# Kernel tuning notes

Measured on AMD Instinct MI355X. Metric: run time of the kernel, lower is better.

Reference implementation:

```python
import jax, jax.numpy as jnp
import numpy as np

SR = 48000
NC = 8      # num_cylinders
NH = 64     # num_harmonics
NB = 32     # num_noisebands
B_, T_ = 2, 65536
TWO_PI = 2.0 * np.pi


def _gumbel_softmax_hard(key, logits, tau=1.0):
    g = jax.random.gumbel(key, logits.shape, dtype=logits.dtype)
    y = jax.nn.softmax((logits + g) / tau)
    hard = jax.nn.one_hot(jnp.argmax(y, axis=-1), logits.shape[-1], dtype=y.dtype)
    return hard + y - jax.lax.stop_gradient(y)  # straight-through (hard=True)


def _resonant_activation(x, min_mag):
    return jnp.sign(x) * (min_mag + (1.0 - min_mag) * jnp.abs(jnp.tanh(x)))


def _format_coefficients(one_hot, fb_gain, refl, lowpass, tau):
    shifted = jnp.roll(one_hot, 1, axis=-1)
    refl = jax.nn.sigmoid(refl) if lowpass else jnp.tanh(refl)
    k1 = _resonant_activation(refl[0], tau)
    k2 = _resonant_activation(refl[1], tau)
    a1 = k1 * (1.0 - k2)
    a2 = jnp.clip(k2, -0.999, 0.999)
    a1_bound = 0.999 - jnp.abs(a2)
    a1 = jnp.clip(a1, -a1_bound, a1_bound)
    g = jax.nn.sigmoid(fb_gain[0]) ** 0.45
    return one_hot * (a1 * g) + shifted * (a2 * g)


def _sample_wise_lpc(x, a):
    # All-pole IIR: y[t] = x[t] - sum_{i=1..P} a[t, i-1] * y[t-i]
    # x: (B,T), a: (B,T,P) -> (B,T). Inherently sequential scan over T.
    B, T = x.shape
    P = a.shape[-1]

    def step(buf, inp):          # buf: (B,P) = [y[t-1], ..., y[t-P]]
        xt, at = inp             # (B,), (B,P)
        yt = xt - jnp.sum(at * buf, axis=-1)
        buf = jnp.concatenate([yt[:, None], buf[:, :-1]], axis=1)
        return buf, yt

    buf0 = jnp.zeros((B, P), x.dtype)
    _, y = jax.lax.scan(step, buf0, (x.T, jnp.transpose(a, (1, 0, 2))))
    return y.T


def _resonator(excitation, delay_param, fb_gain, refl, min_delay, max_delay, lowpass, tau, key):
    # excitation: (B,1,T)
    sel = _gumbel_softmax_hard(key, delay_param)                 # (max-min,)
    coeffs = _format_coefficients(sel, fb_gain, refl, lowpass, tau)
    coeffs = jnp.concatenate([jnp.zeros(min_delay, coeffs.dtype), coeffs])  # (max_delay,)
    x = excitation[:, 0, :]
    B, T = x.shape
    a = jnp.broadcast_to(coeffs[None, None, :], (B, T, max_delay))
    return _sample_wise_lpc(x, a)[:, None, :]


def setup_inputs() -> dict:
    key = jax.random.key(0)
    ks = jax.random.split(key, 16)
    inp = {
        'f0': jax.random.uniform(ks[0], (B_, 1, T_), jnp.float32),
        'harmonic_amplitudes': jax.random.uniform(ks[1], (B_, NC * NH, T_), jnp.float32),
        'harmonic_fm': jax.random.uniform(ks[2], (B_, 1, T_), jnp.float32),
        'cylinder_phase_offsets': jax.random.normal(ks[3], (B_, NC, T_), jnp.float32),
        'cylinder_pulse_shapes': jax.random.uniform(ks[4], (B_, 2 * NC, T_), jnp.float32),
        'noisebank_amplitudes': jax.random.uniform(ks[5], (B_, NB, T_), jnp.float32),
        'noise_pulse_shapes': jax.random.uniform(ks[6], (B_, 2, T_), jnp.float32),
        'noise_pulse_gain': jax.random.uniform(ks[7], (B_, 1, T_), jnp.float32),
        'flow_noise_gain': jax.random.uniform(ks[8], (B_, 1, T_), jnp.float32),
        'noise_bands': jax.random.normal(ks[9], (NB, T_), jnp.float32),
        'delay_a': jax.random.normal(ks[10], (125 - 40,), jnp.float32),
        'fbgain_a': jnp.ones((1,), jnp.float32),
        'refl_a': jax.random.normal(ks[11], (2,), jnp.float32),
        'delay_b': jax.random.normal(ks[12], (125 - 40,), jnp.float32),
        'fbgain_b': jnp.ones((1,), jnp.float32),
        'refl_b': jax.random.normal(ks[13], (2,), jnp.float32),
        'delay_c': jax.random.normal(ks[14], (40 - 32,), jnp.float32),
        'fbgain_c': jnp.ones((1,), jnp.float32),
        'refl_c': jax.random.normal(ks[15], (2,), jnp.float32),
    }
    return inp


def reference(f0, harmonic_amplitudes, harmonic_fm, cylinder_phase_offsets,
              cylinder_pulse_shapes, noisebank_amplitudes, noise_pulse_shapes,
              noise_pulse_gain, flow_noise_gain, noise_bands,
              delay_a, fbgain_a, refl_a, delay_b, fbgain_b, refl_b,
              delay_c, fbgain_c, refl_c):
    B, C, T = cylinder_phase_offsets.shape
    firing_order = jnp.array([0, 4, 3, 7, 5, 2, 6, 1], dtype=f0.dtype)[:NC]
    firing_angles = firing_order / NC * TWO_PI                         # (8,)
    power_cycle_phase = jnp.cumsum(TWO_PI * f0 / SR, axis=-1) * 0.5    # (B,1,T)
    cylinder_phases = (power_cycle_phase + firing_angles[None, :, None]) % TWO_PI  # (B,8,T)

    hp = (cylinder_phases / TWO_PI) ** harmonic_fm                     # (B,8,T)
    hp = hp * TWO_PI
    harm_idx = jnp.arange(1, NH + 1, dtype=hp.dtype)
    osc = -jnp.sin(hp[:, :, None, :] * harm_idx[None, None, :, None])  # (B,8,64,T)
    amps = harmonic_amplitudes.reshape(B, NC, NH, T)
    harmonics = jnp.sum(osc * amps, axis=2)                            # (B,8,T)

    cyl_alpha = cylinder_pulse_shapes[:, :NC, :]
    cyl_beta = cylinder_pulse_shapes[:, NC:, :]
    cyl_env = (1.0 - jnp.exp(-cyl_alpha * cylinder_phases)) * jnp.exp(-cyl_beta * cylinder_phases)
    harmonics = harmonics * cyl_env * 10.0

    # NoiseBank: fixed noise bands weighted per-sample and summed over bands
    noise = jnp.einsum('bnt,nt->bt', noisebank_amplitudes, noise_bands)[:, None, :]  # (B,1,T)

    n_alpha = noise_pulse_shapes[:, 0:1, :]
    n_beta = noise_pulse_shapes[:, 1:2, :]
    noise_phase = power_cycle_phase % TWO_PI
    noise_env = (1.0 - jnp.exp(-n_alpha * noise_phase)) * jnp.exp(-n_beta * noise_phase)
    noise_bursts = noise * noise_env * noise_pulse_gain
    flow_noise = noise * flow_noise_gain * 0.3
    turbulence = harmonics * noise * (noise_pulse_gain + flow_noise_gain) * 0.7
    cylinders = harmonics + noise_bursts + flow_noise + turbulence     # (B,8,T)

    bank_a = jnp.sum(cylinders[:, :4, :], axis=1, keepdims=True)       # (B,1,T)
    bank_b = jnp.sum(cylinders[:, 4:, :], axis=1, keepdims=True)

    ka, kb, kc = jax.random.split(jax.random.key(42), 3)
    res_a = _resonator(bank_a, delay_a, fbgain_a, refl_a, 40, 125, False, 0.0, ka)
    res_b = _resonator(bank_b, delay_b, fbgain_b, refl_b, 40, 125, False, 0.0, kb)
    res_c = _resonator(res_a + res_b, delay_c, fbgain_c, refl_c, 32, 40, True, 0.0, kc)
    return jnp.sum(res_c, axis=1, keepdims=True)                       # (B,1,T)
```

## Files before the change

### kernel.cpp

```cpp
#include <hip/hip_runtime.h>
#include <cstdint>
#include <cstddef>

#define T_ 65536

__device__ __forceinline__ void tf2x32(uint32_t k0, uint32_t k1,
                                       uint32_t& x0, uint32_t& x1) {
  const uint32_t ks[3] = {k0, k1, k0 ^ k1 ^ 0x1BD11BDAu};
  const int R[8] = {13, 15, 26, 6, 17, 29, 16, 24};
  x0 += ks[0]; x1 += ks[1];
#pragma unroll
  for (int i = 0; i < 5; ++i) {
#pragma unroll
    for (int j = 0; j < 4; ++j) {
      const int r = R[(i & 1) * 4 + j];
      x0 += x1;
      x1 = (x1 << r) | (x1 >> (32 - r));
      x1 ^= x0;
    }
    x0 += ks[(i + 1) % 3];
    x1 += ks[(i + 2) % 3] + (uint32_t)(i + 1);
  }
}

__device__ __forceinline__ float gumbel_from_bits(uint32_t b) {
  float u = __uint_as_float((b >> 9) | 0x3f800000u) - 1.0f;
  u = fmaxf(u, 1.17549435e-38f);
  return -logf(-logf(u));
}

__global__ __launch_bounds__(1024) void pcp_coef_kernel(
    const float* __restrict__ f0, float* __restrict__ pcp,
    const float* __restrict__ da, const float* __restrict__ fa, const float* __restrict__ ra,
    const float* __restrict__ db, const float* __restrict__ fb, const float* __restrict__ rb,
    const float* __restrict__ dc, const float* __restrict__ fc, const float* __restrict__ rc,
    float* __restrict__ cws) {
  __shared__ double sm[1024];
  __shared__ float z[128];
  if (blockIdx.x < 2) {
    const int b = blockIdx.x;
    const int tid = threadIdx.x;
    const float* src = f0 + (size_t)b * T_;
    const int base = tid * 64;
    double loc = 0.0;
#pragma unroll 4
    for (int k = 0; k < 16; ++k) {
      const float4 a = *(const float4*)(src + base + 4 * k);
      loc += 6.283185307179586 * (double)a.x / 48000.0;
      loc += 6.283185307179586 * (double)a.y / 48000.0;
      loc += 6.283185307179586 * (double)a.z / 48000.0;
      loc += 6.283185307179586 * (double)a.w / 48000.0;
    }
    sm[tid] = loc;
    __syncthreads();
    for (int off = 1; off < 1024; off <<= 1) {
      double v = (tid >= off) ? sm[tid - off] : 0.0;
      __syncthreads();
      sm[tid] += v;
      __syncthreads();
    }
    double run = (tid > 0) ? sm[tid - 1] : 0.0;
    float* dst = pcp + (size_t)b * T_;
#pragma unroll 4
    for (int k = 0; k < 16; ++k) {
      const float4 a = *(const float4*)(src + base + 4 * k);
      const double r0 = run + 6.283185307179586 * (double)a.x / 48000.0;
      const double r1 = r0  + 6.283185307179586 * (double)a.y / 48000.0;
      const double r2 = r1  + 6.283185307179586 * (double)a.z / 48000.0;
      const double r3 = r2  + 6.283185307179586 * (double)a.w / 48000.0;
      *(float4*)(dst + base + 4 * k) = make_float4((float)(r0 * 0.5), (float)(r1 * 0.5),
                                                   (float)(r2 * 0.5), (float)(r3 * 0.5));
      run = r3;
    }
  } else {
    uint32_t keys[3][2];
#pragma unroll
    for (int q = 0; q < 3; ++q) {
      uint32_t x0 = 0u, x1 = (uint32_t)q;
      tf2x32(0u, 42u, x0, x1);
      keys[q][0] = x0; keys[q][1] = x1;
    }
    const float* dl[3] = {da, db, dc};
    const float* fg[3] = {fa, fb, fc};
    const float* rf[3] = {ra, rb, rc};
    const int Ls[3] = {85, 85, 8};
    const int md[3] = {40, 40, 32};
    const int i = threadIdx.x;
    for (int r = 0; r < 3; ++r) {
      const int L = Ls[r];
      if (i < 128) z[i] = -3.4e38f;
      __syncthreads();
      if (i < L) {
        uint32_t x0 = 0u, x1 = (uint32_t)i;
        tf2x32(keys[r][0], keys[r][1], x0, x1);
        z[i] = dl[r][i] + gumbel_from_bits(x0 ^ x1);
      }
      __syncthreads();
      if (i == 0) {
        int p = 0; float best = z[0];
        for (int j = 1; j < L; ++j) { float v = z[j]; if (v > best) { best = v; p = j; } }
        const bool lowpass = (r == 2);
        float r0 = rf[r][0], r1 = rf[r][1];
        if (lowpass) { r0 = 1.f / (1.f + expf(-r0)); r1 = 1.f / (1.f + expf(-r1)); }
        else         { r0 = tanhf(r0);               r1 = tanhf(r1); }
        const float k1 = tanhf(r0), k2 = tanhf(r1);
        float a1 = k1 * (1.f - k2);
        const float a2 = fminf(fmaxf(k2, -0.999f), 0.999f);
        const float bnd = 0.999f - fabsf(a2);
        a1 = fminf(fmaxf(a1, -bnd), bnd);
        const float g = powf(1.f / (1.f + expf(-fg[r][0])), 0.45f);
        const int D1 = md[r] + p + 1;
        const int D2 = md[r] + ((p + 1) % L) + 1;
        const float C1 = a1 * g;
        const float C2 = a2 * g;
        float* cw = cws + r * 32;
        const float bin4[5] = {1.f, 4.f, 6.f, 4.f, 1.f};
        const float c1p[5] = {1.f, C1, C1*C1, C1*C1*C1, C1*C1*C1*C1};
        const float c2p[5] = {1.f, C2, C2*C2, C2*C2*C2, C2*C2*C2*C2};
        for (int j = 0; j < 5; ++j) {
          cw[j]     = (float)((4 - j) * D1 + j * D2);
          cw[5 + j] = bin4[j] * c1p[4 - j] * c2p[j];
        }
        const int   fd[9] = {D1, D2, 2*D1, D1+D2, 2*D2, 3*D1, 2*D1+D2, D1+2*D2, 3*D2};
        const float fn[9] = {-C1, -C2, C1*C1, 2.f*C1*C2, C2*C2,
                             -C1*C1*C1, -3.f*C1*C1*C2, -3.f*C1*C2*C2, -C2*C2*C2};
        for (int k = 0; k < 9; ++k) {
          cw[10 + k] = (float)fd[k];
          cw[19 + k] = fn[k];
        }
      }
      __syncthreads();
    }
  }
}

__global__ __launch_bounds__(256) void synth_kernel(
    const float* __restrict__ amps,
    const float* __restrict__ fmg,
    const float* __restrict__ cps,
    const float* __restrict__ nba,
    const float* __restrict__ nps,
    const float* __restrict__ npg,
    const float* __restrict__ fng,
    const float* __restrict__ bands,
    const float* __restrict__ pcp,
    float* __restrict__ bank_a, float* __restrict__ bank_b) {
  const float TPF = 6.283185307179586f;
  const int lane = threadIdx.x & 63;
  const int g    = threadIdx.x >> 6;
  const int blk  = blockIdx.x;
  const int b    = blk >> 8;
  const int t    = (blk & 255) * 256 + lane * 4;
  const size_t bt = (size_t)b * T_ + t;

  __shared__ float4 redN[4][64];
  __shared__ float4 redH[4][64];

  const float4 p4 = *(const float4*)(pcp + bt);
  const float4 f4 = *(const float4*)(fmg + bt);

  float4 nse = make_float4(0.f, 0.f, 0.f, 0.f);
#pragma unroll
  for (int j = 0; j < 8; ++j) {
    const int n = g * 8 + j;
    const float4 a = *(const float4*)(nba + ((size_t)b * 32 + n) * T_ + t);
    const float4 w = *(const float4*)(bands + (size_t)n * T_ + t);
    nse.x += a.x * w.x; nse.y += a.y * w.y;
    nse.z += a.z * w.z; nse.w += a.w * w.w;
  }
  redN[g][lane] = nse;

  const int order[8] = {0, 4, 3, 7, 5, 2, 6, 1};
  float4 hp = make_float4(0.f, 0.f, 0.f, 0.f);
#pragma unroll
  for (int cc = 0; cc < 2; ++cc) {
    const int c = 2 * g + cc;
    const float ang = ((float)order[c] / 8.0f) * TPF;
#define SETUP(C_)                                                     \
    float s##C_ = p4.C_ + ang; if (s##C_ >= TPF) s##C_ -= TPF;        \
    float sn##C_, cs##C_;                                             \
    sincosf(TPF * powf(s##C_ / TPF, f4.C_), &sn##C_, &cs##C_);        \
    float sp##C_ = 0.f, sc##C_ = sn##C_;                              \
    const float tc##C_ = 2.f * cs##C_;                                \
    float acc##C_ = 0.f;
    SETUP(x) SETUP(y) SETUP(z) SETUP(w)
#undef SETUP
    const float* ap = amps + ((size_t)b * 512 + (size_t)c * 64) * T_ + t;
#pragma unroll 4
    for (int h = 0; h < 64; ++h) {
      const float4 a = *(const float4*)(ap + (size_t)h * T_);
#define HSTEP(C_) {                                                   \
      acc##C_ += a.C_ * sc##C_;                                       \
      const float nx = tc##C_ * sc##C_ - sp##C_;                      \
      sp##C_ = sc##C_; sc##C_ = nx; }
      HSTEP(x) HSTEP(y) HSTEP(z) HSTEP(w)
#undef HSTEP
    }
    const float4 al = *(const float4*)(cps + ((size_t)b * 16 + c) * T_ + t);
    const float4 be = *(const float4*)(cps + ((size_t)b * 16 + 8 + c) * T_ + t);
#define ENVACC(C_) {                                                  \
      const float env = (1.f - expf(-al.C_ * s##C_)) * expf(-be.C_ * s##C_); \
      hp.C_ += -acc##C_ * env * 10.f; }
    ENVACC(x) ENVACC(y) ENVACC(z) ENVACC(w)
#undef ENVACC
  }
  redH[g][lane] = hp;
  __syncthreads();

  if (g == 0) {
    const float4 nA = redN[0][lane], nB = redN[1][lane],
                 nC = redN[2][lane], nD = redN[3][lane];
    const float4 hA0 = redH[0][lane], hA1 = redH[1][lane],
                 hB0 = redH[2][lane], hB1 = redH[3][lane];
    const float4 g4  = *(const float4*)(npg + bt);
    const float4 fl4 = *(const float4*)(fng + bt);
    const float4 na4 = *(const float4*)(nps + (size_t)b * 2 * T_ + t);
    const float4 nb4 = *(const float4*)(nps + ((size_t)b * 2 + 1) * T_ + t);
    float4 outA, outB;
#define FIN(C_) {                                                     \
    const float nse = nA.C_ + nB.C_ + nC.C_ + nD.C_;                  \
    const float ha = hA0.C_ + hA1.C_;                                 \
    const float hb = hB0.C_ + hB1.C_;                                 \
    float q = p4.C_; if (q >= TPF) q -= TPF;                          \
    const float ne = (1.f - expf(-na4.C_ * q)) * expf(-nb4.C_ * q);   \
    const float com = nse * (ne * g4.C_ + fl4.C_ * 0.3f);             \
    const float K = nse * (g4.C_ + fl4.C_) * 0.7f;                    \
    outA.C_ = ha * (1.f + K) + 4.f * com;                             \
    outB.C_ = hb * (1.f + K) + 4.f * com; }
    FIN(x) FIN(y) FIN(z) FIN(w)
#undef FIN
    *(float4*)(bank_a + bt) = outA;
    *(float4*)(bank_b + bt) = outB;
  }
}

__global__ __launch_bounds__(256) void prep_ab_kernel(
    const float* __restrict__ BA, const float* __restrict__ BB,
    const float* __restrict__ CW, float* __restrict__ XA, float* __restrict__ XB) {
  const int idx = blockIdx.x * 256 + threadIdx.x;
  const int t = idx & (T_ - 1);
  const int s = idx >> 16;
  const int r = s >> 1, b = s & 1;
  const float* xin = (r == 0 ? BA : BB) + (size_t)b * T_;
  float* xout = (r == 0 ? XA : XB) + (size_t)b * T_;
  const float* cw = CW + r * 32;
  float acc = xin[t];
#pragma unroll
  for (int k = 0; k < 9; ++k) {
    const int d = (int)cw[10 + k];
    const float n = cw[19 + k];
    const int tc = t - d;
    const float u = xin[tc >= 0 ? tc : 0];
    acc += (tc >= 0) ? n * u : 0.f;
  }
  xout[t] = acc;
}

__global__ __launch_bounds__(256) void prep_c_kernel(
    const float* __restrict__ RA, const float* __restrict__ RB,
    const float* __restrict__ CW, float* __restrict__ XC) {
  const int idx = blockIdx.x * 256 + threadIdx.x;
  const int t = idx & (T_ - 1);
  const int b = idx >> 16;
  const float* ya = RA + (size_t)b * T_;
  const float* yb = RB + (size_t)b * T_;
  const float* cw = CW + 64;
  float acc = ya[t] + yb[t];
#pragma unroll
  for (int k = 0; k < 9; ++k) {
    const int d = (int)cw[10 + k];
    const float n = cw[19 + k];
    const int tc = t - d;
    const float u = ya[tc >= 0 ? tc : 0] + yb[tc >= 0 ? tc : 0];
    acc += (tc >= 0) ? n * u : 0.f;
  }
  XC[idx] = acc;
}

__device__ __forceinline__ void gld16(const float* g, float* l) {
  __builtin_amdgcn_global_load_lds((const __attribute__((address_space(1))) void*)g,
                                   (__attribute__((address_space(3))) void*)l, 16, 0, 0);
}

__device__ __forceinline__ void poly_scan(const float* __restrict__ x,
                                          float* __restrict__ y,
                                          const float* __restrict__ cf,
                                          float* __restrict__ sm) {
  const int o = threadIdx.x & 63;
  const int e0 = (int)cf[0], e1 = (int)cf[1], e2 = (int)cf[2],
            e3 = (int)cf[3], e4 = (int)cf[4];
  const float fc0 = cf[5], fc1 = cf[6], fc2 = cf[7], fc3 = cf[8], fc4 = cf[9];
  float* ring = sm;
  float* st   = sm + 1024;

#pragma unroll
  for (int i = 0; i < 16; ++i) ring[o + i * 64] = 0.f;

#pragma unroll
  for (int seg = 0; seg < 2; ++seg) {
    const float* g = x + seg * 1024 + (o << 2);
    float* l = st + seg * 1024;
    gld16(g, l); gld16(g + 256, l + 256);
    gld16(g + 512, l + 512); gld16(g + 768, l + 768);
  }
  asm volatile("s_waitcnt vmcnt(4)" ::: "memory");
  __builtin_amdgcn_sched_barrier(0);

  float a0 = ring[(o - e0) & 1023];
  float a1v = ring[(o - e1) & 1023];
  float a2v = ring[(o - e2) & 1023];
  float a3v = ring[(o - e3) & 1023];
  float a4v = ring[(o - e4) & 1023];
  float b0 = ring[(o + 64 - e0) & 1023];
  float b1v = ring[(o + 64 - e1) & 1023];
  float b2v = ring[(o + 64 - e2) & 1023];
  float b3v = ring[(o + 64 - e3) & 1023];
  float b4v = ring[(o + 64 - e4) & 1023];

  int m = 0;
  for (int ph = 0; ph < 64; ++ph) {
    if (ph < 62) {
      const int seg = ph + 2;
      const float* g = x + seg * 1024 + (o << 2);
      float* l = st + (seg % 3) * 1024;
      gld16(g, l); gld16(g + 256, l + 256);
      gld16(g + 512, l + 512); gld16(g + 768, l + 768);
    }
    const float* bq = st + (ph % 3) * 1024;
    float xv0 = bq[o];
    float xv1 = bq[64 + o];
#pragma unroll
    for (int li = 0; li < 8; ++li) {
      const float sA = fmaf(fc0, a0, fc1 * a1v) + fmaf(fc2, a2v, fc3 * a3v);
      const float y0 = xv0 + fmaf(fc4, a4v, sA);
      ring[(m + o) & 1023] = y0;
      const float sB = fmaf(fc0, b0, fc1 * b1v) + fmaf(fc2, b2v, fc3 * b3v);
      const float y1 = xv1 + fmaf(fc4, b4v, sB);
      ring[(m + 64 + o) & 1023] = y1;
      a0  = ring[(m + 128 + o - e0) & 1023];
      a1v = ring[(m + 128 + o - e1) & 1023];
      a2v = ring[(m + 128 + o - e2) & 1023];
      a3v = ring[(m + 128 + o - e3) & 1023];
      a4v = ring[(m + 128 + o - e4) & 1023];
      b0  = ring[(m + 192 + o - e0) & 1023];
      b1v = ring[(m + 192 + o - e1) & 1023];
      b2v = ring[(m + 192 + o - e2) & 1023];
      b3v = ring[(m + 192 + o - e3) & 1023];
      b4v = ring[(m + 192 + o - e4) & 1023];
      if (li < 7) { xv0 = bq[(li + 1) * 128 + o]; xv1 = bq[(li + 1) * 128 + 64 + o]; }
      m += 128;
    }
#pragma unroll
    for (int j = 0; j < 4; ++j) {
      const float4 v = *(const float4*)(ring + (o << 2) + j * 256);
      *(float4*)(y + ph * 1024 + j * 256 + (o << 2)) = v;
    }
    asm volatile("s_waitcnt vmcnt(8)" ::: "memory");
    __builtin_amdgcn_sched_barrier(0);
  }
}

__global__ __launch_bounds__(64) void res_ab_kernel(
    const float* __restrict__ XA, const float* __restrict__ XB,
    float* __restrict__ RA, float* __restrict__ RB, const float* __restrict__ CW) {
  __shared__ float sm[4096];
  const int r = blockIdx.x >> 1;
  const int b = blockIdx.x & 1;
  poly_scan((r == 0 ? XA : XB) + (size_t)b * T_,
            (r == 0 ? RA : RB) + (size_t)b * T_, CW + r * 32, sm);
}

__global__ __launch_bounds__(64) void res_c_kernel(
    const float* __restrict__ XC, float* __restrict__ out,
    const float* __restrict__ CW) {
  __shared__ float sm[4096];
  poly_scan(XC + (size_t)blockIdx.x * T_, out + (size_t)blockIdx.x * T_,
            CW + 64, sm);
}

extern "C" void kernel_launch(void* const* d_in, const int* in_sizes, int n_in,
                              void* d_out, int out_size, void* d_ws, size_t ws_size,
                              hipStream_t stream) {
  const float* f0    = (const float*)d_in[0];
  const float* amps  = (const float*)d_in[1];
  const float* fmg   = (const float*)d_in[2];
  const float* cps   = (const float*)d_in[4];
  const float* nba   = (const float*)d_in[5];
  const float* nps   = (const float*)d_in[6];
  const float* npg   = (const float*)d_in[7];
  const float* fng   = (const float*)d_in[8];
  const float* bands = (const float*)d_in[9];
  const float* da  = (const float*)d_in[10];
  const float* fga = (const float*)d_in[11];
  const float* ra  = (const float*)d_in[12];
  const float* db  = (const float*)d_in[13];
  const float* fgb = (const float*)d_in[14];
  const float* rb  = (const float*)d_in[15];
  const float* dc  = (const float*)d_in[16];
  const float* fgc = (const float*)d_in[17];
  const float* rc  = (const float*)d_in[18];
  float* out = (float*)d_out;
  float* ws  = (float*)d_ws;

  float* S0 = ws;
  float* S1 = ws + 131072;
  float* S2 = ws + 262144;
  float* S3 = ws + 393216;
  float* CW = ws + 524288;

  pcp_coef_kernel<<<3, 1024, 0, stream>>>(f0, S0, da, fga, ra, db, fgb, rb,
                                          dc, fgc, rc, CW);
  synth_kernel<<<512, 256, 0, stream>>>(amps, fmg, cps, nba, nps, npg, fng, bands,
                                        S0, S1, S2);
  prep_ab_kernel<<<1024, 256, 0, stream>>>(S1, S2, CW, S0, S3);
  res_ab_kernel<<<4, 64, 0, stream>>>(S0, S3, S1, S2, CW);
  prep_c_kernel<<<512, 256, 0, stream>>>(S1, S2, CW, S3);
  res_c_kernel<<<2, 64, 0, stream>>>(S3, out, CW);
}
```

Baseline: 248.7 us.

## Fuse FIR prep into scan kernels with producer warps feeding LDS double buffer

Removes the separate prep_ab and prep_c kernels. Three producer wavefronts now compute the 9-tap FIR pre-filter for the next 1024-sample segment into a double-buffered LDS area, while wavefront 0 runs the sequential scan on the current one, with the two sides synchronised by __syncthreads each phase. This drops two launches and the intermediate global round trip. In exchange it adds a block barrier per segment, and the producers make uncoalesced scalar gathers that may not keep pace with the scan.

Result: slower. 578.7 us (+132.7%).

```diff
diff --git a/kernel.cpp b/kernel.cpp
--- a/kernel.cpp
+++ b/kernel.cpp
@@ -234,148 +234,124 @@
   }
 }
 
-__global__ __launch_bounds__(256) void prep_ab_kernel(
-    const float* __restrict__ BA, const float* __restrict__ BB,
-    const float* __restrict__ CW, float* __restrict__ XA, float* __restrict__ XB) {
-  const int idx = blockIdx.x * 256 + threadIdx.x;
-  const int t = idx & (T_ - 1);
-  const int s = idx >> 16;
-  const int r = s >> 1, b = s & 1;
-  const float* xin = (r == 0 ? BA : BB) + (size_t)b * T_;
-  float* xout = (r == 0 ? XA : XB) + (size_t)b * T_;
-  const float* cw = CW + r * 32;
-  float acc = xin[t];
-#pragma unroll
-  for (int k = 0; k < 9; ++k) {
-    const int d = (int)cw[10 + k];
-    const float n = cw[19 + k];
-    const int tc = t - d;
-    const float u = xin[tc >= 0 ? tc : 0];
-    acc += (tc >= 0) ? n * u : 0.f;
-  }
-  xout[t] = acc;
-}
-
-__global__ __launch_bounds__(256) void prep_c_kernel(
-    const float* __restrict__ RA, const float* __restrict__ RB,
-    const float* __restrict__ CW, float* __restrict__ XC) {
-  const int idx = blockIdx.x * 256 + threadIdx.x;
-  const int t = idx & (T_ - 1);
-  const int b = idx >> 16;
-  const float* ya = RA + (size_t)b * T_;
-  const float* yb = RB + (size_t)b * T_;
-  const float* cw = CW + 64;
-  float acc = ya[t] + yb[t];
-#pragma unroll
-  for (int k = 0; k < 9; ++k) {
-    const int d = (int)cw[10 + k];
-    const float n = cw[19 + k];
-    const int tc = t - d;
-    const float u = ya[tc >= 0 ? tc : 0] + yb[tc >= 0 ? tc : 0];
-    acc += (tc >= 0) ? n * u : 0.f;
-  }
-  XC[idx] = acc;
-}
-
-__device__ __forceinline__ void gld16(const float* g, float* l) {
-  __builtin_amdgcn_global_load_lds((const __attribute__((address_space(1))) void*)g,
-                                   (__attribute__((address_space(3))) void*)l, 16, 0, 0);
-}
-
-__device__ __forceinline__ void poly_scan(const float* __restrict__ x,
-                                          float* __restrict__ y,
-                                          const float* __restrict__ cf,
-                                          float* __restrict__ sm) {
-  const int o = threadIdx.x & 63;
+template <bool TWO_IN>
+__device__ __forceinline__ void fused_scan(const float* __restrict__ x1,
+                                           const float* __restrict__ x2,
+                                           float* __restrict__ y,
+                                           const float* __restrict__ cf,
+                                           float* __restrict__ sm) {
+  const int tid = threadIdx.x;
+  const int wid = tid >> 6;
+  const int o = tid & 63;
+  float* ring = sm;
+  float* xb   = sm + 1024;
+
   const int e0 = (int)cf[0], e1 = (int)cf[1], e2 = (int)cf[2],
             e3 = (int)cf[3], e4 = (int)cf[4];
   const float fc0 = cf[5], fc1 = cf[6], fc2 = cf[7], fc3 = cf[8], fc4 = cf[9];
-  float* ring = sm;
-  float* st   = sm + 1024;
-
-#pragma unroll
-  for (int i = 0; i < 16; ++i) ring[o + i * 64] = 0.f;
-
-#pragma unroll
-  for (int seg = 0; seg < 2; ++seg) {
-    const float* g = x + seg * 1024 + (o << 2);
-    float* l = st + seg * 1024;
-    gld16(g, l); gld16(g + 256, l + 256);
-    gld16(g + 512, l + 512); gld16(g + 768, l + 768);
-  }
-  asm volatile("s_waitcnt vmcnt(4)" ::: "memory");
-  __builtin_amdgcn_sched_barrier(0);
-
-  float a0 = ring[(o - e0) & 1023];
-  float a1v = ring[(o - e1) & 1023];
-  float a2v = ring[(o - e2) & 1023];
-  float a3v = ring[(o - e3) & 1023];
-  float a4v = ring[(o - e4) & 1023];
-  float b0 = ring[(o + 64 - e0) & 1023];
-  float b1v = ring[(o + 64 - e1) & 1023];
-  float b2v = ring[(o + 64 - e2) & 1023];
-  float b3v = ring[(o + 64 - e3) & 1023];
-  float b4v = ring[(o + 64 - e4) & 1023];
+  int   fd[9];
+  float fn[9];
+#pragma unroll
+  for (int k = 0; k < 9; ++k) { fd[k] = (int)cf[10 + k]; fn[k] = cf[19 + k]; }
+
+#define PRODUCE(BASE)                                                         \
+  {                                                                           \
+    const int tid1 = tid - 64;                                                \
+    float* dst = xb + (((BASE) >> 10) & 1) * 1024;                            \
+    for (int s = tid1; s < 256; s += 192) {                                   \
+      const int t0 = (BASE) + 4 * s;                                          \
+      float4 xv = *(const float4*)(x1 + t0);                                  \
+      if (TWO_IN) { const float4 w = *(const float4*)(x2 + t0);               \
+        xv.x += w.x; xv.y += w.y; xv.z += w.z; xv.w += w.w; }                 \
+      float c0 = xv.x, c1 = xv.y, c2 = xv.z, c3 = xv.w;                       \
+      _Pragma("unroll")                                                       \
+      for (int k = 0; k < 9; ++k) {                                           \
+        const int d = fd[k]; const float n = fn[k];                           \
+        { const int tc = t0 + 0 - d; float u = x1[tc >= 0 ? tc : 0];          \
+          if (TWO_IN) u += x2[tc >= 0 ? tc : 0];                              \
+          c0 += (tc >= 0) ? n * u : 0.f; }                                    \
+        { const int tc = t0 + 1 - d; float u = x1[tc >= 0 ? tc : 0];          \
+          if (TWO_IN) u += x2[tc >= 0 ? tc : 0];                              \
+          c1 += (tc >= 0) ? n * u : 0.f; }                                    \
+        { const int tc = t0 + 2 - d; float u = x1[tc >= 0 ? tc : 0];          \
+          if (TWO_IN) u += x2[tc >= 0 ? tc : 0];                              \
+          c2 += (tc >= 0) ? n * u : 0.f; }                                    \
+        { const int tc = t0 + 3 - d; float u = x1[tc >= 0 ? tc : 0];          \
+          if (TWO_IN) u += x2[tc >= 0 ? tc : 0];                              \
+          c3 += (tc >= 0) ? n * u : 0.f; }                                    \
+      }                                                                       \
+      *(float4*)(dst + 4 * s) = make_float4(c0, c1, c2, c3);                  \
+    }                                                                         \
+  }
+
+  if (wid == 0) {
+#pragma unroll
+    for (int i = 0; i < 16; ++i) ring[o + i * 64] = 0.f;
+  } else {
+    PRODUCE(0)
+  }
+  __syncthreads();
+
+  float a0 = 0.f, a1v = 0.f, a2v = 0.f, a3v = 0.f, a4v = 0.f;
+  float b0 = 0.f, b1v = 0.f, b2v = 0.f, b3v = 0.f, b4v = 0.f;
 
   int m = 0;
   for (int ph = 0; ph < 64; ++ph) {
-    if (ph < 62) {
-      const int seg = ph + 2;
-      const float* g = x + seg * 1024 + (o << 2);
-      float* l = st + (seg % 3) * 1024;
-      gld16(g, l); gld16(g + 256, l + 256);
-      gld16(g + 512, l + 512); gld16(g + 768, l + 768);
-    }
-    const float* bq = st + (ph % 3) * 1024;
-    float xv0 = bq[o];
-    float xv1 = bq[64 + o];
-#pragma unroll
-    for (int li = 0; li < 8; ++li) {
-      const float sA = fmaf(fc0, a0, fc1 * a1v) + fmaf(fc2, a2v, fc3 * a3v);
-      const float y0 = xv0 + fmaf(fc4, a4v, sA);
-      ring[(m + o) & 1023] = y0;
-      const float sB = fmaf(fc0, b0, fc1 * b1v) + fmaf(fc2, b2v, fc3 * b3v);
-      const float y1 = xv1 + fmaf(fc4, b4v, sB);
-      ring[(m + 64 + o) & 1023] = y1;
-      a0  = ring[(m + 128 + o - e0) & 1023];
-      a1v = ring[(m + 128 + o - e1) & 1023];
-      a2v = ring[(m + 128 + o - e2) & 1023];
-      a3v = ring[(m + 128 + o - e3) & 1023];
-      a4v = ring[(m + 128 + o - e4) & 1023];
-      b0  = ring[(m + 192 + o - e0) & 1023];
-      b1v = ring[(m + 192 + o - e1) & 1023];
-      b2v = ring[(m + 192 + o - e2) & 1023];
-      b3v = ring[(m + 192 + o - e3) & 1023];
-      b4v = ring[(m + 192 + o - e4) & 1023];
-      if (li < 7) { xv0 = bq[(li + 1) * 128 + o]; xv1 = bq[(li + 1) * 128 + 64 + o]; }
-      m += 128;
-    }
-#pragma unroll
-    for (int j = 0; j < 4; ++j) {
-      const float4 v = *(const float4*)(ring + (o << 2) + j * 256);
-      *(float4*)(y + ph * 1024 + j * 256 + (o << 2)) = v;
-    }
-    asm volatile("s_waitcnt vmcnt(8)" ::: "memory");
-    __builtin_amdgcn_sched_barrier(0);
-  }
-}
-
-__global__ __launch_bounds__(64) void res_ab_kernel(
-    const float* __restrict__ XA, const float* __restrict__ XB,
+    if (wid == 0) {
+      const float* bq = xb + (ph & 1) * 1024;
+      float xv0 = bq[o];
+      float xv1 = bq[64 + o];
+#pragma unroll
+      for (int li = 0; li < 8; ++li) {
+        const float sA = fmaf(fc0, a0, fc1 * a1v) + fmaf(fc2, a2v, fc3 * a3v);
+        const float y0 = xv0 + fmaf(fc4, a4v, sA);
+        ring[(m + o) & 1023] = y0;
+        const float sB = fmaf(fc0, b0, fc1 * b1v) + fmaf(fc2, b2v, fc3 * b3v);
+        const float y1 = xv1 + fmaf(fc4, b4v, sB);
+        ring[(m + 64 + o) & 1023] = y1;
+        a0  = ring[(m + 128 + o - e0) & 1023];
+        a1v = ring[(m + 128 + o - e1) & 1023];
+        a2v = ring[(m + 128 + o - e2) & 1023];
+        a3v = ring[(m + 128 + o - e3) & 1023];
+        a4v = ring[(m + 128 + o - e4) & 1023];
+        b0  = ring[(m + 192 + o - e0) & 1023];
+        b1v = ring[(m + 192 + o - e1) & 1023];
+        b2v = ring[(m + 192 + o - e2) & 1023];
+        b3v = ring[(m + 192 + o - e3) & 1023];
+        b4v = ring[(m + 192 + o - e4) & 1023];
+        if (li < 7) { xv0 = bq[(li + 1) * 128 + o]; xv1 = bq[(li + 1) * 128 + 64 + o]; }
+        m += 128;
+      }
+#pragma unroll
+      for (int j = 0; j < 4; ++j) {
+        const float4 v = *(const float4*)(ring + (o << 2) + j * 256);
+        *(float4*)(y + ph * 1024 + j * 256 + (o << 2)) = v;
+      }
+    } else if (ph + 1 < 64) {
+      PRODUCE((ph + 1) * 1024)
+    }
+    __syncthreads();
+  }
+#undef PRODUCE
+}
+
+__global__ __launch_bounds__(256) void res_ab_kernel(
+    const float* __restrict__ BA, const float* __restrict__ BB,
     float* __restrict__ RA, float* __restrict__ RB, const float* __restrict__ CW) {
-  __shared__ float sm[4096];
+  __shared__ float sm[3072];
   const int r = blockIdx.x >> 1;
   const int b = blockIdx.x & 1;
-  poly_scan((r == 0 ? XA : XB) + (size_t)b * T_,
-            (r == 0 ? RA : RB) + (size_t)b * T_, CW + r * 32, sm);
-}
-
-__global__ __launch_bounds__(64) void res_c_kernel(
-    const float* __restrict__ XC, float* __restrict__ out,
-    const float* __restrict__ CW) {
-  __shared__ float sm[4096];
-  poly_scan(XC + (size_t)blockIdx.x * T_, out + (size_t)blockIdx.x * T_,
-            CW + 64, sm);
+  fused_scan<false>((r == 0 ? BA : BB) + (size_t)b * T_, nullptr,
+                    (r == 0 ? RA : RB) + (size_t)b * T_, CW + r * 32, sm);
+}
+
+__global__ __launch_bounds__(256) void res_c_kernel(
+    const float* __restrict__ RA, const float* __restrict__ RB,
+    float* __restrict__ out, const float* __restrict__ CW) {
+  __shared__ float sm[3072];
+  const int b = blockIdx.x;
+  fused_scan<true>(RA + (size_t)b * T_, RB + (size_t)b * T_,
+                   out + (size_t)b * T_, CW + 64, sm);
 }
 
 extern "C" void kernel_launch(void* const* d_in, const int* in_sizes, int n_in,
@@ -412,8 +388,6 @@
                                           dc, fgc, rc, CW);
   synth_kernel<<<512, 256, 0, stream>>>(amps, fmg, cps, nba, nps, npg, fng, bands,
                                         S0, S1, S2);
-  prep_ab_kernel<<<1024, 256, 0, stream>>>(S1, S2, CW, S0, S3);
-  res_ab_kernel<<<4, 64, 0, stream>>>(S0, S3, S1, S2, CW);
-  prep_c_kernel<<<512, 256, 0, stream>>>(S1, S2, CW, S3);
-  res_c_kernel<<<2, 64, 0, stream>>>(S3, out, CW);
-}
+  res_ab_kernel<<<4, 256, 0, stream>>>(S1, S2, S0, S3, CW);
+  res_c_kernel<<<2, 256, 0, stream>>>(S0, S3, out, CW);
+}
```
